# Kernel tuning notes

Hardware: AMD Instinct MI355X
Metric: run time of the kernel (lower is better)

Reference implementation:

```python
import jax, jax.numpy as jnp
import numpy as np

N = 100000   # nodes
DEG = 32     # in-degree per node
E = N * DEG  # 3.2M edges
D = 24       # node feature dim
NK = 2       # number of anisotropic kernels (tile(...,2) in source forces 2)
H = 64       # MLP hidden/out channels


def setup_inputs() -> dict:
    key = jax.random.key(0)
    k1, k2, k3, k4 = jax.random.split(key, 4)
    x = jax.random.normal(k1, (N, D), dtype=jnp.float32)
    src = jax.random.randint(k2, (E,), 0, N)
    tgt = jnp.repeat(jnp.arange(N), DEG)  # every node has DEG in-edges -> no 0/0
    edge_index = jnp.stack([src, tgt]).astype(jnp.int64)
    kvals = jax.random.normal(k3, (NK, E), dtype=jnp.float32)
    # Linear(2*D -> H, bias=False), xavier-like scale
    W = jax.random.normal(k4, (H, NK * D), dtype=jnp.float32) * (1.0 / (NK * D))
    return {"x": x, "edge_index": edge_index, "kvals": kvals, "W": W}


def reference(x, edge_index, kvals, W):
    src, tgt = edge_index[0], edge_index[1]
    xs = x[src]  # [E, D] gathered source features
    # per-kernel sparse aggregation: out_k[i] = sum_{e: tgt[e]==i} kvals[k,e] * x[src[e]]
    out = jnp.concatenate(
        [jax.ops.segment_sum(kvals[k][:, None] * xs, tgt, num_segments=N)
         for k in range(NK)], axis=1)  # [N, NK*D]
    # adj_norm: subtract tiled neighbor mean
    deg = jax.ops.segment_sum(jnp.ones((E,), x.dtype), tgt, num_segments=N)  # [N]
    sum_x = jax.ops.segment_sum(xs, tgt, num_segments=N)  # [N, D]
    norm_x = sum_x / deg[:, None]
    out = out - jnp.tile(norm_x, (1, NK)) + jnp.tile(x, (1, NK))
    # MLP: single bias-free linear, no activation
    return out @ W.T  # [N, H]
```

## Files before the change

### kernel.cpp

```cpp
#include <hip/hip_runtime.h>


#define NN   100000
#define DEG  32
#define EE   (NN * DEG)
#define DD   24
#define HH   64
#define NPB  32
#define TPB  256
#define NPW  8
#define PST  56

typedef __attribute__((ext_vector_type(8)))  short short8;
typedef __attribute__((ext_vector_type(16))) float float16;

__device__ __forceinline__ unsigned short f2bf(float f) {
    union { float f; unsigned u; } v; v.f = f;
    unsigned r = v.u + 0x7fffu + ((v.u >> 16) & 1u);
    return (unsigned short)(r >> 16);
}

__device__ __forceinline__ float bf2f(unsigned u) {
    union { unsigned i; float f; } v; v.i = u << 16; return v.f;
}

__device__ __forceinline__ unsigned pk(unsigned a, unsigned b) {
    return __builtin_amdgcn_perm(b, a, 0x05040100u);
}

__device__ __forceinline__ short8 mk8(unsigned u0, unsigned u1, unsigned u2, unsigned u3) {
    union { unsigned u[4]; short8 s; } p;
    p.u[0] = u0; p.u[1] = u1; p.u[2] = u2; p.u[3] = u3;
    return p.s;
}

__global__ void xcvt(const float* __restrict__ x, unsigned short* __restrict__ xb, int n4) {
    int i = blockIdx.x * blockDim.x + threadIdx.x;
    if (i < n4) {
        float4 v = ((const float4*)x)[i];
        ushort4 o;
        o.x = f2bf(v.x); o.y = f2bf(v.y); o.z = f2bf(v.z); o.w = f2bf(v.w);
        ((ushort4*)xb)[i] = o;
    }
}

__global__ __launch_bounds__(TPB, 4) void gnn(
    const unsigned short* __restrict__ xb,
    const int*            __restrict__ ei,
    const float*          __restrict__ kv,
    const float*          __restrict__ W,
    float*                __restrict__ out)
{
    __shared__ int            ei_s[NPB * DEG];
    __shared__ unsigned short kv_s[2 * NPB * DEG];
    __shared__ unsigned short pre_s[NPB * PST];

    const int t    = threadIdx.x;
    const int lane = t & 63;
    const int w    = t >> 6;
    const int m    = lane & 31;
    const int kh   = lane >> 5;
    const int kh8  = kh * 8;
    const int base = blockIdx.x * NPB;
    const int dclamp = (m < DD) ? m : (DD - 1);
    const int m2     = dclamp * 2;
    const char* xbc  = (const char*)xb;

    {
        const size_t eb = (size_t)base * DEG;
        int4 ev = ((const int4*)(ei + eb))[t];
        ev.x *= 48; ev.y *= 48; ev.z *= 48; ev.w *= 48;
        ((int4*)ei_s)[t] = ev;
        const float4 c0 = ((const float4*)(kv + eb))[t];
        const float4 c1 = ((const float4*)(kv + EE + eb))[t];
        ushort4 u0, u1;
        u0.x = f2bf(c0.x); u0.y = f2bf(c0.y); u0.z = f2bf(c0.z); u0.w = f2bf(c0.w);
        u1.x = f2bf(c1.x); u1.y = f2bf(c1.y); u1.z = f2bf(c1.z); u1.w = f2bf(c1.w);
        ((ushort4*)kv_s)[t] = u0;
        ((ushort4*)(kv_s + NPB * DEG))[t] = u1;
    }
    __syncthreads();

    const unsigned short* kvrow = kv_s + (m & 1) * (NPB * DEG);

    unsigned g[2][16];
    unsigned xv[2];

    #define LOAD_NODE(nl, sl) do {                                             \
        const int el_ = (nl) * DEG + kh8;                                      \
        const int4 s0_ = *(const int4*)(ei_s + el_);                           \
        const int4 s1_ = *(const int4*)(ei_s + el_ + 4);                       \
        const int4 s2_ = *(const int4*)(ei_s + el_ + 16);                      \
        const int4 s3_ = *(const int4*)(ei_s + el_ + 20);                      \
        g[sl][0]  = *(const unsigned short*)(xbc + (unsigned)(s0_.x + m2));    \
        g[sl][1]  = *(const unsigned short*)(xbc + (unsigned)(s0_.y + m2));    \
        g[sl][2]  = *(const unsigned short*)(xbc + (unsigned)(s0_.z + m2));    \
        g[sl][3]  = *(const unsigned short*)(xbc + (unsigned)(s0_.w + m2));    \
        g[sl][4]  = *(const unsigned short*)(xbc + (unsigned)(s1_.x + m2));    \
        g[sl][5]  = *(const unsigned short*)(xbc + (unsigned)(s1_.y + m2));    \
        g[sl][6]  = *(const unsigned short*)(xbc + (unsigned)(s1_.z + m2));    \
        g[sl][7]  = *(const unsigned short*)(xbc + (unsigned)(s1_.w + m2));    \
        g[sl][8]  = *(const unsigned short*)(xbc + (unsigned)(s2_.x + m2));    \
        g[sl][9]  = *(const unsigned short*)(xbc + (unsigned)(s2_.y + m2));    \
        g[sl][10] = *(const unsigned short*)(xbc + (unsigned)(s2_.z + m2));    \
        g[sl][11] = *(const unsigned short*)(xbc + (unsigned)(s2_.w + m2));    \
        g[sl][12] = *(const unsigned short*)(xbc + (unsigned)(s3_.x + m2));    \
        g[sl][13] = *(const unsigned short*)(xbc + (unsigned)(s3_.y + m2));    \
        g[sl][14] = *(const unsigned short*)(xbc + (unsigned)(s3_.z + m2));    \
        g[sl][15] = *(const unsigned short*)(xbc + (unsigned)(s3_.w + m2));    \
        xv[sl] = xb[(base + (nl)) * DD + dclamp];                              \
    } while (0)

    LOAD_NODE(w * NPW, 0);

    #pragma unroll
    for (int i = 0; i < NPW; ++i) {
        const int cur = i & 1;
        const int nl  = w * NPW + i;
        if (i < NPW - 1) LOAD_NODE(nl + 1, cur ^ 1);

        const int el = nl * DEG + kh8;
        const short8 raw0 = *(const short8*)(kvrow + el);
        const short8 raw1 = *(const short8*)(kvrow + el + 16);
        const unsigned fill = (m == 2) ? 0x3F803F80u : 0u;
        const short8 af0 = (m < 2) ? raw0 : mk8(fill, fill, fill, fill);
        const short8 af1 = (m < 2) ? raw1 : mk8(fill, fill, fill, fill);

        const short8 bf0 = mk8(pk(g[cur][0],  g[cur][1]),  pk(g[cur][2],  g[cur][3]),
                               pk(g[cur][4],  g[cur][5]),  pk(g[cur][6],  g[cur][7]));
        const short8 bf1 = mk8(pk(g[cur][8],  g[cur][9]),  pk(g[cur][10], g[cur][11]),
                               pk(g[cur][12], g[cur][13]), pk(g[cur][14], g[cur][15]));

        float16 acc;
        #pragma unroll
        for (int r = 0; r < 16; ++r) acc[r] = 0.f;
        acc = __builtin_amdgcn_mfma_f32_32x32x16_bf16(af0, bf0, acc, 0, 0, 0);
        acc = __builtin_amdgcn_mfma_f32_32x32x16_bf16(af1, bf1, acc, 0, 0, 0);

        if (kh == 0 && m < DD) {
            const float sm = acc[2] * (1.f / 32.f);
            const float pv = bf2f(xv[cur]) - sm;
            pre_s[nl * PST + m]      = f2bf(acc[0] + pv);
            pre_s[nl * PST + 24 + m] = f2bf(acc[1] + pv);
        }
    }
    #undef LOAD_NODE
    __syncthreads();

    if (w < 2) {
        const int h = w * 32 + m;

        float16 acc;
        #pragma unroll
        for (int r = 0; r < 16; ++r) acc[r] = 0.f;

        #pragma unroll
        for (int kc = 0; kc < 3; ++kc) {
            const int c0 = kc * 16 + kh8;
            const short8 af = *(const short8*)(pre_s + m * PST + c0);
            const float* wr = W + h * 48 + c0;
            const float4 wA = ((const float4*)wr)[0];
            const float4 wB = ((const float4*)wr)[1];
            const short8 bf = mk8(pk(f2bf(wA.x), f2bf(wA.y)), pk(f2bf(wA.z), f2bf(wA.w)),
                                  pk(f2bf(wB.x), f2bf(wB.y)), pk(f2bf(wB.z), f2bf(wB.w)));
            acc = __builtin_amdgcn_mfma_f32_32x32x16_bf16(af, bf, acc, 0, 0, 0);
        }

        #pragma unroll
        for (int r = 0; r < 16; ++r) {
            const int row = (r & 3) + 8 * (r >> 2) + 4 * kh;
            out[(size_t)(base + row) * HH + h] = acc[r];
        }
    }
}

extern "C" void kernel_launch(void* const* d_in, const int* in_sizes, int n_in,
                              void* d_out, int out_size, void* d_ws, size_t ws_size,
                              hipStream_t stream) {
    const float* x  = (const float*)d_in[0];
    const int*   ei = (const int*)d_in[1];
    const float* kv = (const float*)d_in[2];
    const float* W  = (const float*)d_in[3];
    float* out = (float*)d_out;

    unsigned short* xb = (unsigned short*)d_ws;
    const int n4 = NN * DD / 4;
    xcvt<<<(n4 + 255) / 256, 256, 0, stream>>>(x, xb, n4);

    const int grid = NN / NPB;
    gnn<<<grid, TPB, 0, stream>>>(xb, ei, kv, W, out);
}
```

Baseline: 127.2 us.

## Gather neighbor features via global_load_lds into double-buffered LDS tiles

Replaces the per-lane 2-byte register gathers of neighbor rows with 4-byte direct global-to-LDS loads (global_load_lds), each covering a whole 48-byte source row with 12 lanes. Tiles are double-buffered per wave and synchronised with manual vmcnt waits. The self feature rows are also staged into LDS once per block. The aim is fewer, wider gather instructions and less register pressure from prefetching. In exchange it adds LDS traffic for the transpose reads, and the hand-coded waitcnt values must match the number of loads in flight.

```diff
diff --git a/kernel.cpp b/kernel.cpp
--- a/kernel.cpp
+++ b/kernel.cpp
@@ -34,6 +34,12 @@
     return p.s;
 }
 
+__device__ __forceinline__ void gl_lds4(const void* g, void* l) {
+    __builtin_amdgcn_global_load_lds(
+        (const __attribute__((address_space(1))) void*)g,
+        (__attribute__((address_space(3))) void*)l, 4, 0, 0);
+}
+
 __global__ void xcvt(const float* __restrict__ x, unsigned short* __restrict__ xb, int n4) {
     int i = blockIdx.x * blockDim.x + threadIdx.x;
     if (i < n4) {
@@ -53,7 +59,9 @@
 {
     __shared__ int            ei_s[NPB * DEG];
     __shared__ unsigned short kv_s[2 * NPB * DEG];
+    __shared__ unsigned short xv_s[NPB * DD];
     __shared__ unsigned short pre_s[NPB * PST];
+    __shared__ __align__(16) char tiles[4][2][2048];
 
     const int t    = threadIdx.x;
     const int lane = t & 63;
@@ -61,10 +69,10 @@
     const int m    = lane & 31;
     const int kh   = lane >> 5;
     const int kh8  = kh * 8;
+    const int t4   = lane >> 4;
+    const int dsl  = lane & 15;
     const int base = blockIdx.x * NPB;
-    const int dclamp = (m < DD) ? m : (DD - 1);
-    const int m2     = dclamp * 2;
-    const char* xbc  = (const char*)xb;
+    const char* xbc = (const char*)xb;
 
     {
         const size_t eb = (size_t)base * DEG;
@@ -78,46 +86,49 @@
         u1.x = f2bf(c1.x); u1.y = f2bf(c1.y); u1.z = f2bf(c1.z); u1.w = f2bf(c1.w);
         ((ushort4*)kv_s)[t] = u0;
         ((ushort4*)(kv_s + NPB * DEG))[t] = u1;
+        if (t < (NPB * DD) / 4)
+            ((ushort4*)xv_s)[t] = ((const ushort4*)(xb + (size_t)base * DD))[t];
     }
     __syncthreads();
 
     const unsigned short* kvrow = kv_s + (m & 1) * (NPB * DEG);
+    const int n0 = w * NPW;
 
-    unsigned g[2][16];
-    unsigned xv[2];
-
-    #define LOAD_NODE(nl, sl) do {                                             \
-        const int el_ = (nl) * DEG + kh8;                                      \
-        const int4 s0_ = *(const int4*)(ei_s + el_);                           \
-        const int4 s1_ = *(const int4*)(ei_s + el_ + 4);                       \
-        const int4 s2_ = *(const int4*)(ei_s + el_ + 16);                      \
-        const int4 s3_ = *(const int4*)(ei_s + el_ + 20);                      \
-        g[sl][0]  = *(const unsigned short*)(xbc + (unsigned)(s0_.x + m2));    \
-        g[sl][1]  = *(const unsigned short*)(xbc + (unsigned)(s0_.y + m2));    \
-        g[sl][2]  = *(const unsigned short*)(xbc + (unsigned)(s0_.z + m2));    \
-        g[sl][3]  = *(const unsigned short*)(xbc + (unsigned)(s0_.w + m2));    \
-        g[sl][4]  = *(const unsigned short*)(xbc + (unsigned)(s1_.x + m2));    \
-        g[sl][5]  = *(const unsigned short*)(xbc + (unsigned)(s1_.y + m2));    \
-        g[sl][6]  = *(const unsigned short*)(xbc + (unsigned)(s1_.z + m2));    \
-        g[sl][7]  = *(const unsigned short*)(xbc + (unsigned)(s1_.w + m2));    \
-        g[sl][8]  = *(const unsigned short*)(xbc + (unsigned)(s2_.x + m2));    \
-        g[sl][9]  = *(const unsigned short*)(xbc + (unsigned)(s2_.y + m2));    \
-        g[sl][10] = *(const unsigned short*)(xbc + (unsigned)(s2_.z + m2));    \
-        g[sl][11] = *(const unsigned short*)(xbc + (unsigned)(s2_.w + m2));    \
-        g[sl][12] = *(const unsigned short*)(xbc + (unsigned)(s3_.x + m2));    \
-        g[sl][13] = *(const unsigned short*)(xbc + (unsigned)(s3_.y + m2));    \
-        g[sl][14] = *(const unsigned short*)(xbc + (unsigned)(s3_.z + m2));    \
-        g[sl][15] = *(const unsigned short*)(xbc + (unsigned)(s3_.w + m2));    \
-        xv[sl] = xb[(base + (nl)) * DD + dclamp];                              \
+    #define ISSUE(nl) do {                                                     \
+        char* tb_ = tiles[w][(nl) & 1];                                        \
+        _Pragma("unroll")                                                      \
+        for (int i_ = 0; i_ < 8; ++i_) {                                       \
+            const int eo_ = ei_s[(nl) * DEG + i_ * 4 + t4];                    \
+            const char* gp_ = (dsl < 12) ? (xbc + (unsigned)(eo_ + dsl * 4))   \
+                                         : xbc;                                \
+            gl_lds4(gp_, tb_ + i_ * 256);                                      \
+        }                                                                      \
     } while (0)
 
-    LOAD_NODE(w * NPW, 0);
+    ISSUE(n0);
 
     #pragma unroll
-    for (int i = 0; i < NPW; ++i) {
-        const int cur = i & 1;
-        const int nl  = w * NPW + i;
-        if (i < NPW - 1) LOAD_NODE(nl + 1, cur ^ 1);
+    for (int p = 0; p < NPW; ++p) {
+        const int nl = n0 + p;
+        if (p < NPW - 1) {
+            ISSUE(nl + 1);
+            __builtin_amdgcn_s_waitcnt(0xF78);
+        } else {
+            __builtin_amdgcn_s_waitcnt(0xF70);
+        }
+
+        const unsigned short* tile = (const unsigned short*)tiles[w][p & 1];
+
+        unsigned r0 = tile[(kh8 + 0) * 32 + m], r1 = tile[(kh8 + 1) * 32 + m];
+        unsigned r2 = tile[(kh8 + 2) * 32 + m], r3 = tile[(kh8 + 3) * 32 + m];
+        unsigned r4 = tile[(kh8 + 4) * 32 + m], r5 = tile[(kh8 + 5) * 32 + m];
+        unsigned r6 = tile[(kh8 + 6) * 32 + m], r7 = tile[(kh8 + 7) * 32 + m];
+        const short8 bf0 = mk8(pk(r0, r1), pk(r2, r3), pk(r4, r5), pk(r6, r7));
+        unsigned s0 = tile[(16 + kh8 + 0) * 32 + m], s1 = tile[(16 + kh8 + 1) * 32 + m];
+        unsigned s2 = tile[(16 + kh8 + 2) * 32 + m], s3 = tile[(16 + kh8 + 3) * 32 + m];
+        unsigned s4 = tile[(16 + kh8 + 4) * 32 + m], s5 = tile[(16 + kh8 + 5) * 32 + m];
+        unsigned s6 = tile[(16 + kh8 + 6) * 32 + m], s7 = tile[(16 + kh8 + 7) * 32 + m];
+        const short8 bf1 = mk8(pk(s0, s1), pk(s2, s3), pk(s4, s5), pk(s6, s7));
 
         const int el = nl * DEG + kh8;
         const short8 raw0 = *(const short8*)(kvrow + el);
@@ -125,11 +136,6 @@
         const unsigned fill = (m == 2) ? 0x3F803F80u : 0u;
         const short8 af0 = (m < 2) ? raw0 : mk8(fill, fill, fill, fill);
         const short8 af1 = (m < 2) ? raw1 : mk8(fill, fill, fill, fill);
-
-        const short8 bf0 = mk8(pk(g[cur][0],  g[cur][1]),  pk(g[cur][2],  g[cur][3]),
-                               pk(g[cur][4],  g[cur][5]),  pk(g[cur][6],  g[cur][7]));
-        const short8 bf1 = mk8(pk(g[cur][8],  g[cur][9]),  pk(g[cur][10], g[cur][11]),
-                               pk(g[cur][12], g[cur][13]), pk(g[cur][14], g[cur][15]));
 
         float16 acc;
         #pragma unroll
@@ -139,12 +145,12 @@
 
         if (kh == 0 && m < DD) {
             const float sm = acc[2] * (1.f / 32.f);
-            const float pv = bf2f(xv[cur]) - sm;
+            const float pv = bf2f((unsigned)xv_s[nl * DD + m]) - sm;
             pre_s[nl * PST + m]      = f2bf(acc[0] + pv);
             pre_s[nl * PST + 24 + m] = f2bf(acc[1] + pv);
         }
     }
-    #undef LOAD_NODE
+    #undef ISSUE
     __syncthreads();
 
     if (w < 2) {
```

Measured after the change: 130.1 us. 1.02x slower.
